# Performance work log

Hardware: AMD Instinct MI355X
Metric: run time of the kernel (lower is better)

Reference implementation:

```python
import jax, jax.numpy as jnp
import numpy as np

NEG_SLOPE = 0.2


def setup_inputs() -> dict:
    key = jax.random.key(0)
    ks = jax.random.split(key, 5)
    N, E, Din, Dout = 100000, 1600000, 64, 64
    x = jax.random.normal(ks[0], (N, Din), dtype=jnp.float32)
    edge_index = jax.random.randint(ks[1], (2, E), 0, N, dtype=jnp.int64)
    # Glorot-ish scale for weights
    W_l = jax.random.normal(ks[2], (Din, Dout), dtype=jnp.float32) / np.sqrt(Din)
    W_r = jax.random.normal(ks[3], (Din, Dout), dtype=jnp.float32) / np.sqrt(Din)
    att = jax.random.normal(ks[4], (Dout,), dtype=jnp.float32) / np.sqrt(Dout)
    bias = jnp.zeros((Dout,), dtype=jnp.float32)
    return {"x": x, "edge_index": edge_index, "W_l": W_l, "W_r": W_r, "att": att, "bias": bias}


def reference(x, edge_index, W_l, W_r, att, bias):
    N = x.shape[0]
    # PyG GATv2Conv default: add self loops
    loop = jnp.arange(N, dtype=edge_index.dtype)
    src = jnp.concatenate([edge_index[0], loop])  # j (source / message)
    dst = jnp.concatenate([edge_index[1], loop])  # i (target / aggregation)

    x_l = x @ W_l  # [N, Dout] source transform
    x_r = x @ W_r  # [N, Dout] target transform

    # per-edge attention logit: att . LeakyReLU(x_l[j] + x_r[i])
    e = jax.nn.leaky_relu(x_l[src] + x_r[dst], NEG_SLOPE) @ att  # [E+N]

    # segment softmax grouped by destination node
    e_max = jax.ops.segment_max(e, dst, num_segments=N)  # [N]
    e_exp = jnp.exp(e - e_max[dst])
    denom = jax.ops.segment_sum(e_exp, dst, num_segments=N)  # [N]
    alpha = e_exp / denom[dst]  # [E+N]

    # weighted scatter-add aggregation of source features
    out = jax.ops.segment_sum(alpha[:, None] * x_l[src], dst, num_segments=N)
    return out + bias
```

## Files before the change

### kernel.cpp

```cpp
#include <hip/hip_runtime.h>
#include <hip/hip_fp16.h>

#define NEG_SLOPE 0.2f
#define CH 4096
#define UN 16
#define BW 512
#define CAP2 10240
#define QCAP 2560

__global__ __launch_bounds__(256) void k_gemm(const float* __restrict__ x,
                                              const float* __restrict__ Wl,
                                              const float* __restrict__ Wr,
                                              __half* __restrict__ xl,
                                              __half* __restrict__ xr,
                                              int* __restrict__ bcount,
                                              int NB, int N) {
    __shared__ float sX[128 * 64];
    __shared__ float sW[64 * 128];
    const int t = threadIdx.x;
    const int B = blockIdx.x * 128;

    if (blockIdx.x == 0 && t < NB) bcount[t] = 0;

    for (int f = t; f < 2048; f += 256) {
        const int k = f >> 5, cg = f & 31;
        float4 v;
        if (cg < 16) v = reinterpret_cast<const float4*>(Wl)[k * 16 + cg];
        else         v = reinterpret_cast<const float4*>(Wr)[k * 16 + (cg - 16)];
        reinterpret_cast<float4*>(sW)[f] = v;
    }
    for (int f = t; f < 2048; f += 256) {
        const int r = B + (f >> 4);
        float4 v = {0.f, 0.f, 0.f, 0.f};
        if (r < N) v = reinterpret_cast<const float4*>(x)[(size_t)B * 16 + f];
        reinterpret_cast<float4*>(sX)[f] = v;
    }
    __syncthreads();

    const int cg = t & 31;
    const int g  = t >> 5;

    float4 acc[16];
#pragma unroll
    for (int i = 0; i < 16; i++) acc[i] = make_float4(0.f, 0.f, 0.f, 0.f);

    for (int kk = 0; kk < 64; kk += 4) {
        const float4 w0 = reinterpret_cast<const float4*>(sW)[(kk + 0) * 32 + cg];
        const float4 w1 = reinterpret_cast<const float4*>(sW)[(kk + 1) * 32 + cg];
        const float4 w2 = reinterpret_cast<const float4*>(sW)[(kk + 2) * 32 + cg];
        const float4 w3 = reinterpret_cast<const float4*>(sW)[(kk + 3) * 32 + cg];
#pragma unroll
        for (int i = 0; i < 16; i++) {
            const float4 xv = reinterpret_cast<const float4*>(sX)[(g * 16 + i) * 16 + (kk >> 2)];
            acc[i].x = fmaf(xv.x, w0.x, acc[i].x);
            acc[i].y = fmaf(xv.x, w0.y, acc[i].y);
            acc[i].z = fmaf(xv.x, w0.z, acc[i].z);
            acc[i].w = fmaf(xv.x, w0.w, acc[i].w);
            acc[i].x = fmaf(xv.y, w1.x, acc[i].x);
            acc[i].y = fmaf(xv.y, w1.y, acc[i].y);
            acc[i].z = fmaf(xv.y, w1.z, acc[i].z);
            acc[i].w = fmaf(xv.y, w1.w, acc[i].w);
            acc[i].x = fmaf(xv.z, w2.x, acc[i].x);
            acc[i].y = fmaf(xv.z, w2.y, acc[i].y);
            acc[i].z = fmaf(xv.z, w2.z, acc[i].z);
            acc[i].w = fmaf(xv.z, w2.w, acc[i].w);
            acc[i].x = fmaf(xv.w, w3.x, acc[i].x);
            acc[i].y = fmaf(xv.w, w3.y, acc[i].y);
            acc[i].z = fmaf(xv.w, w3.z, acc[i].z);
            acc[i].w = fmaf(xv.w, w3.w, acc[i].w);
        }
    }

    const int c = cg * 4;
    __half* dstp = (c < 64) ? (xl + c) : (xr + (c - 64));
#pragma unroll
    for (int i = 0; i < 16; i++) {
        const int r = B + g * 16 + i;
        if (r < N) {
            __half2 h01, h23;
            h01.x = __float2half_rn(acc[i].x);
            h01.y = __float2half_rn(acc[i].y);
            h23.x = __float2half_rn(acc[i].z);
            h23.y = __float2half_rn(acc[i].w);
            uint2 u;
            u.x = *reinterpret_cast<unsigned int*>(&h01);
            u.y = *reinterpret_cast<unsigned int*>(&h23);
            *reinterpret_cast<uint2*>(dstp + (size_t)r * 64) = u;
        }
    }
}

__global__ __launch_bounds__(256) void k_part(const int* __restrict__ src,
                                              const int* __restrict__ dst,
                                              int* __restrict__ bcount,
                                              int* __restrict__ part,
                                              int E, int M, int NB) {
    __shared__ int skey[CH];
    __shared__ unsigned char sbkt[CH];
    __shared__ int hist[256];
    __shared__ int lcur[256];
    __shared__ int gofs[256];
    const int t = threadIdx.x;
    const int b = blockIdx.x;
    const int lo = b * CH;
    const int cnt = min(M - lo, CH);

    hist[t] = 0;
    __syncthreads();

    int rs[UN], rd[UN];
#pragma unroll
    for (int u = 0; u < UN; u++) {
        const int k = lo + t + u * 256;
        rd[u] = -1; rs[u] = 0;
        if (k < M) {
            if (k < E) { rs[u] = src[k]; rd[u] = dst[k]; }
            else       { rs[u] = k - E;  rd[u] = rs[u]; }
        }
    }
#pragma unroll
    for (int u = 0; u < UN; u++)
        if (rd[u] >= 0) atomicAdd(&hist[rd[u] >> 9], 1);
    __syncthreads();

    const int h = hist[t];
    lcur[t] = h;
    __syncthreads();
    for (int o = 1; o < 256; o <<= 1) {
        const int v = (t >= o) ? lcur[t - o] : 0;
        __syncthreads();
        lcur[t] += v;
        __syncthreads();
    }
    const int ex = lcur[t] - h;
    int gbase = 0;
    if (t < NB && h > 0) gbase = atomicAdd(&bcount[t], h);
    __syncthreads();
    lcur[t] = ex;
    gofs[t] = t * CAP2 + gbase - ex;
    __syncthreads();

#pragma unroll
    for (int u = 0; u < UN; u++) {
        if (rd[u] >= 0) {
            const int bkt = rd[u] >> 9;
            const int p = atomicAdd(&lcur[bkt], 1);
            skey[p] = (rs[u] << 9) | (rd[u] & 511);
            sbkt[p] = (unsigned char)bkt;
        }
    }
    __syncthreads();

    for (int i = t; i < cnt; i += 256) {
        const int bkt = sbkt[i];
        const int pos = gofs[bkt] + i;
        if (pos - bkt * CAP2 < CAP2) part[pos] = skey[i];
    }
}

__global__ __launch_bounds__(256) void k_bsf(const int* __restrict__ part,
                                             const int* __restrict__ bcount,
                                             int* __restrict__ sedge,
                                             int* __restrict__ off,
                                             int* __restrict__ deg, int N) {
    __shared__ int skey[QCAP];
    __shared__ int outk[QCAP];
    __shared__ int lhist[128];
    __shared__ int loff[128];
    __shared__ int lcur[128];
    __shared__ int sh2[128];
    __shared__ int scnt;
    const int t = threadIdx.x;
    const int bkt = blockIdx.x >> 2;
    const int qt  = blockIdx.x & 3;
    const int base  = bkt * CAP2;
    const int qbase = base + qt * QCAP;
    const int n = min(bcount[bkt], CAP2);

    if (t == 0) scnt = 0;
    if (t < 128) lhist[t] = 0;
    __syncthreads();

    for (int i = t; i < n; i += 256) {
        const int k = part[base + i];
        const int dl = k & 511;
        if ((dl >> 7) == qt) {
            const int p = atomicAdd(&scnt, 1);
            if (p < QCAP) {
                skey[p] = k;
                atomicAdd(&lhist[dl & 127], 1);
            }
        }
    }
    __syncthreads();
    const int m = min(scnt, QCAP);

    if (t < 128) sh2[t] = lhist[t];
    __syncthreads();
    for (int o = 1; o < 128; o <<= 1) {
        int v = 0;
        if (t < 128 && t >= o) v = sh2[t - o];
        __syncthreads();
        if (t < 128) sh2[t] += v;
        __syncthreads();
    }
    if (t < 128) {
        const int ex = sh2[t] - lhist[t];
        loff[t] = ex;
        lcur[t] = ex;
        const int node = (bkt << 9) + (qt << 7) + t;
        if (node < N) { off[node] = qbase + ex; deg[node] = lhist[t]; }
    }
    __syncthreads();

    for (int i = t; i < m; i += 256) {
        const int k = skey[i];
        const int pos = atomicAdd(&lcur[k & 127], 1);
        outk[pos] = k >> 9;
    }
    __syncthreads();
    for (int i = t; i < m; i += 256) sedge[qbase + i] = outk[i];
}

__global__ void k_fused(const int* __restrict__ offv, const int* __restrict__ degv,
                        const int* __restrict__ sedge, const __half* __restrict__ xl,
                        const __half* __restrict__ xr, const float* __restrict__ att,
                        const float* __restrict__ bias, float* __restrict__ out, int N) {
    const int lane = threadIdx.x & 63;
    const int gl = lane & 15;
    const int q = lane >> 4;
    int wave = (blockIdx.x * blockDim.x + threadIdx.x) >> 6;
    const int nw = (gridDim.x * blockDim.x) >> 6;
    const float4 a = reinterpret_cast<const float4*>(att)[gl];
    const float4 b = reinterpret_cast<const float4*>(bias)[gl];
    for (int i = wave; i < N; i += nw) {
        const int base = offv[i];
        const int dg = degv[i];
        const uint2 xru = reinterpret_cast<const uint2*>(xr + (size_t)i * 64)[gl];
        const float2 r01 = __half22float2(*reinterpret_cast<const __half2*>(&xru.x));
        const float2 r23 = __half22float2(*reinterpret_cast<const __half2*>(&xru.y));
        float s = 0.f;
        float4 acc = {0.f, 0.f, 0.f, 0.f};
        int tt = q;
        for (; tt + 4 < dg; tt += 8) {
            const int j0 = sedge[base + tt];
            const int j1 = sedge[base + tt + 4];
            const uint2 xu0 = reinterpret_cast<const uint2*>(xl + (size_t)j0 * 64)[gl];
            const uint2 xu1 = reinterpret_cast<const uint2*>(xl + (size_t)j1 * 64)[gl];
            const float2 l01a = __half22float2(*reinterpret_cast<const __half2*>(&xu0.x));
            const float2 l23a = __half22float2(*reinterpret_cast<const __half2*>(&xu0.y));
            const float2 l01b = __half22float2(*reinterpret_cast<const __half2*>(&xu1.x));
            const float2 l23b = __half22float2(*reinterpret_cast<const __half2*>(&xu1.y));
            float v0 = l01a.x + r01.x; v0 = fmaxf(v0, NEG_SLOPE * v0);
            float v1 = l01a.y + r01.y; v1 = fmaxf(v1, NEG_SLOPE * v1);
            float v2 = l23a.x + r23.x; v2 = fmaxf(v2, NEG_SLOPE * v2);
            float v3 = l23a.y + r23.y; v3 = fmaxf(v3, NEG_SLOPE * v3);
            float u0 = l01b.x + r01.x; u0 = fmaxf(u0, NEG_SLOPE * u0);
            float u1 = l01b.y + r01.y; u1 = fmaxf(u1, NEG_SLOPE * u1);
            float u2 = l23b.x + r23.x; u2 = fmaxf(u2, NEG_SLOPE * u2);
            float u3 = l23b.y + r23.y; u3 = fmaxf(u3, NEG_SLOPE * u3);
            float p0 = a.x * v0 + a.y * v1 + a.z * v2 + a.w * v3;
            float p1 = a.x * u0 + a.y * u1 + a.z * u2 + a.w * u3;
            p0 += __shfl_xor(p0, 1, 16);
            p1 += __shfl_xor(p1, 1, 16);
            p0 += __shfl_xor(p0, 2, 16);
            p1 += __shfl_xor(p1, 2, 16);
            p0 += __shfl_xor(p0, 4, 16);
            p1 += __shfl_xor(p1, 4, 16);
            p0 += __shfl_xor(p0, 8, 16);
            p1 += __shfl_xor(p1, 8, 16);
            const float w0 = __expf(p0);
            const float w1 = __expf(p1);
            s += w0 + w1;
            acc.x = fmaf(w0, l01a.x, acc.x); acc.x = fmaf(w1, l01b.x, acc.x);
            acc.y = fmaf(w0, l01a.y, acc.y); acc.y = fmaf(w1, l01b.y, acc.y);
            acc.z = fmaf(w0, l23a.x, acc.z); acc.z = fmaf(w1, l23b.x, acc.z);
            acc.w = fmaf(w0, l23a.y, acc.w); acc.w = fmaf(w1, l23b.y, acc.w);
        }
        for (; tt < dg; tt += 4) {
            const int j = sedge[base + tt];
            const uint2 xu = reinterpret_cast<const uint2*>(xl + (size_t)j * 64)[gl];
            const float2 l01 = __half22float2(*reinterpret_cast<const __half2*>(&xu.x));
            const float2 l23 = __half22float2(*reinterpret_cast<const __half2*>(&xu.y));
            float v0 = l01.x + r01.x; v0 = fmaxf(v0, NEG_SLOPE * v0);
            float v1 = l01.y + r01.y; v1 = fmaxf(v1, NEG_SLOPE * v1);
            float v2 = l23.x + r23.x; v2 = fmaxf(v2, NEG_SLOPE * v2);
            float v3 = l23.y + r23.y; v3 = fmaxf(v3, NEG_SLOPE * v3);
            float p = a.x * v0 + a.y * v1 + a.z * v2 + a.w * v3;
            p += __shfl_xor(p, 1, 16);
            p += __shfl_xor(p, 2, 16);
            p += __shfl_xor(p, 4, 16);
            p += __shfl_xor(p, 8, 16);
            const float w = __expf(p);
            s += w;
            acc.x = fmaf(w, l01.x, acc.x);
            acc.y = fmaf(w, l01.y, acc.y);
            acc.z = fmaf(w, l23.x, acc.z);
            acc.w = fmaf(w, l23.y, acc.w);
        }
        s += __shfl_xor(s, 16); s += __shfl_xor(s, 32);
        acc.x += __shfl_xor(acc.x, 16); acc.x += __shfl_xor(acc.x, 32);
        acc.y += __shfl_xor(acc.y, 16); acc.y += __shfl_xor(acc.y, 32);
        acc.z += __shfl_xor(acc.z, 16); acc.z += __shfl_xor(acc.z, 32);
        acc.w += __shfl_xor(acc.w, 16); acc.w += __shfl_xor(acc.w, 32);
        if (q == 0) {
            const float inv = 1.f / s;
            float4 o;
            o.x = fmaf(acc.x, inv, b.x);
            o.y = fmaf(acc.y, inv, b.y);
            o.z = fmaf(acc.z, inv, b.z);
            o.w = fmaf(acc.w, inv, b.w);
            reinterpret_cast<float4*>(out)[(size_t)i * 16 + gl] = o;
        }
    }
}

extern "C" void kernel_launch(void* const* d_in, const int* in_sizes, int n_in,
                              void* d_out, int out_size, void* d_ws, size_t ws_size,
                              hipStream_t stream) {
    const float* x    = (const float*)d_in[0];
    const int*   ei   = (const int*)d_in[1];
    const float* Wl   = (const float*)d_in[2];
    const float* Wr   = (const float*)d_in[3];
    const float* att  = (const float*)d_in[4];
    const float* bias = (const float*)d_in[5];
    float* out = (float*)d_out;

    const int N = in_sizes[0] / 64;
    const int E = in_sizes[1] / 2;
    const int M = E + N;
    const int ng  = (N + 127) / 128;
    const int nch = (M + CH - 1) / CH;
    const int NB  = (N + BW - 1) / BW;

    __half* xl = (__half*)d_ws;
    __half* xr = xl + (size_t)N * 64;
    int* deg    = (int*)(xr + (size_t)N * 64);
    int* off    = deg + N;
    int* bcount = off + N;
    int* part   = bcount + NB;
    int* sedge  = part + (size_t)NB * CAP2;

    k_gemm<<<ng, 256, 0, stream>>>(x, Wl, Wr, xl, xr, bcount, NB, N);
    k_part<<<nch, 256, 0, stream>>>(ei, ei + E, bcount, part, E, M, NB);
    k_bsf<<<NB * 4, 256, 0, stream>>>(part, bcount, sedge, off, deg, N);
    k_fused<<<2048, 256, 0, stream>>>(off, deg, sedge, xl, xr, att, bias, out, N);
}
```

Before: 206.0 us.

## Merge GEMM and edge partition into one launch; warp-aggregate bucket-split atomics

The node-feature GEMM and the edge partition pass are merged into a single kernel that picks its role from the block index, with a shared 64KB buffer reused by both branches. The bucket counters are now zeroed with an async memset, since the partition blocks may run alongside the GEMM blocks. This lets two independent stages overlap and removes one launch boundary. In the bucket-split kernel, per-thread shared atomics on the key counter are replaced by a warp ballot with one atomic per warp. The cost is higher shared memory use for the partition blocks, which can lower their occupancy, plus an extra memset launch.

```diff
diff --git a/kernel.cpp b/kernel.cpp
--- a/kernel.cpp
+++ b/kernel.cpp
@@ -8,153 +8,151 @@
 #define CAP2 10240
 #define QCAP 2560
 
-__global__ __launch_bounds__(256) void k_gemm(const float* __restrict__ x,
-                                              const float* __restrict__ Wl,
-                                              const float* __restrict__ Wr,
-                                              __half* __restrict__ xl,
-                                              __half* __restrict__ xr,
-                                              int* __restrict__ bcount,
-                                              int NB, int N) {
-    __shared__ float sX[128 * 64];
-    __shared__ float sW[64 * 128];
+__global__ __launch_bounds__(256) void k_gp(const float* __restrict__ x,
+                                            const float* __restrict__ Wl,
+                                            const float* __restrict__ Wr,
+                                            __half* __restrict__ xl,
+                                            __half* __restrict__ xr,
+                                            const int* __restrict__ src,
+                                            const int* __restrict__ dst,
+                                            int* __restrict__ bcount,
+                                            int* __restrict__ part,
+                                            int E, int M, int NB, int ng, int N) {
+    __shared__ float smem[16384];
     const int t = threadIdx.x;
-    const int B = blockIdx.x * 128;
-
-    if (blockIdx.x == 0 && t < NB) bcount[t] = 0;
-
-    for (int f = t; f < 2048; f += 256) {
-        const int k = f >> 5, cg = f & 31;
-        float4 v;
-        if (cg < 16) v = reinterpret_cast<const float4*>(Wl)[k * 16 + cg];
-        else         v = reinterpret_cast<const float4*>(Wr)[k * 16 + (cg - 16)];
-        reinterpret_cast<float4*>(sW)[f] = v;
-    }
-    for (int f = t; f < 2048; f += 256) {
-        const int r = B + (f >> 4);
-        float4 v = {0.f, 0.f, 0.f, 0.f};
-        if (r < N) v = reinterpret_cast<const float4*>(x)[(size_t)B * 16 + f];
-        reinterpret_cast<float4*>(sX)[f] = v;
-    }
-    __syncthreads();
-
-    const int cg = t & 31;
-    const int g  = t >> 5;
-
-    float4 acc[16];
-#pragma unroll
-    for (int i = 0; i < 16; i++) acc[i] = make_float4(0.f, 0.f, 0.f, 0.f);
-
-    for (int kk = 0; kk < 64; kk += 4) {
-        const float4 w0 = reinterpret_cast<const float4*>(sW)[(kk + 0) * 32 + cg];
-        const float4 w1 = reinterpret_cast<const float4*>(sW)[(kk + 1) * 32 + cg];
-        const float4 w2 = reinterpret_cast<const float4*>(sW)[(kk + 2) * 32 + cg];
-        const float4 w3 = reinterpret_cast<const float4*>(sW)[(kk + 3) * 32 + cg];
+
+    if (blockIdx.x < ng) {
+        float* sX = smem;
+        float* sW = smem + 8192;
+        const int B = blockIdx.x * 128;
+
+        for (int f = t; f < 2048; f += 256) {
+            const int k = f >> 5, cg = f & 31;
+            float4 v;
+            if (cg < 16) v = reinterpret_cast<const float4*>(Wl)[k * 16 + cg];
+            else         v = reinterpret_cast<const float4*>(Wr)[k * 16 + (cg - 16)];
+            reinterpret_cast<float4*>(sW)[f] = v;
+        }
+        for (int f = t; f < 2048; f += 256) {
+            const int r = B + (f >> 4);
+            float4 v = {0.f, 0.f, 0.f, 0.f};
+            if (r < N) v = reinterpret_cast<const float4*>(x)[(size_t)B * 16 + f];
+            reinterpret_cast<float4*>(sX)[f] = v;
+        }
+        __syncthreads();
+
+        const int cg = t & 31;
+        const int g  = t >> 5;
+
+        float4 acc[16];
+#pragma unroll
+        for (int i = 0; i < 16; i++) acc[i] = make_float4(0.f, 0.f, 0.f, 0.f);
+
+        for (int kk = 0; kk < 64; kk += 4) {
+            const float4 w0 = reinterpret_cast<const float4*>(sW)[(kk + 0) * 32 + cg];
+            const float4 w1 = reinterpret_cast<const float4*>(sW)[(kk + 1) * 32 + cg];
+            const float4 w2 = reinterpret_cast<const float4*>(sW)[(kk + 2) * 32 + cg];
+            const float4 w3 = reinterpret_cast<const float4*>(sW)[(kk + 3) * 32 + cg];
+#pragma unroll
+            for (int i = 0; i < 16; i++) {
+                const float4 xv = reinterpret_cast<const float4*>(sX)[(g * 16 + i) * 16 + (kk >> 2)];
+                acc[i].x = fmaf(xv.x, w0.x, acc[i].x);
+                acc[i].y = fmaf(xv.x, w0.y, acc[i].y);
+                acc[i].z = fmaf(xv.x, w0.z, acc[i].z);
+                acc[i].w = fmaf(xv.x, w0.w, acc[i].w);
+                acc[i].x = fmaf(xv.y, w1.x, acc[i].x);
+                acc[i].y = fmaf(xv.y, w1.y, acc[i].y);
+                acc[i].z = fmaf(xv.y, w1.z, acc[i].z);
+                acc[i].w = fmaf(xv.y, w1.w, acc[i].w);
+                acc[i].x = fmaf(xv.z, w2.x, acc[i].x);
+                acc[i].y = fmaf(xv.z, w2.y, acc[i].y);
+                acc[i].z = fmaf(xv.z, w2.z, acc[i].z);
+                acc[i].w = fmaf(xv.z, w2.w, acc[i].w);
+                acc[i].x = fmaf(xv.w, w3.x, acc[i].x);
+                acc[i].y = fmaf(xv.w, w3.y, acc[i].y);
+                acc[i].z = fmaf(xv.w, w3.z, acc[i].z);
+                acc[i].w = fmaf(xv.w, w3.w, acc[i].w);
+            }
+        }
+
+        const int c = cg * 4;
+        __half* dstp = (c < 64) ? (xl + c) : (xr + (c - 64));
 #pragma unroll
         for (int i = 0; i < 16; i++) {
-            const float4 xv = reinterpret_cast<const float4*>(sX)[(g * 16 + i) * 16 + (kk >> 2)];
-            acc[i].x = fmaf(xv.x, w0.x, acc[i].x);
-            acc[i].y = fmaf(xv.x, w0.y, acc[i].y);
-            acc[i].z = fmaf(xv.x, w0.z, acc[i].z);
-            acc[i].w = fmaf(xv.x, w0.w, acc[i].w);
-            acc[i].x = fmaf(xv.y, w1.x, acc[i].x);
-            acc[i].y = fmaf(xv.y, w1.y, acc[i].y);
-            acc[i].z = fmaf(xv.y, w1.z, acc[i].z);
-            acc[i].w = fmaf(xv.y, w1.w, acc[i].w);
-            acc[i].x = fmaf(xv.z, w2.x, acc[i].x);
-            acc[i].y = fmaf(xv.z, w2.y, acc[i].y);
-            acc[i].z = fmaf(xv.z, w2.z, acc[i].z);
-            acc[i].w = fmaf(xv.z, w2.w, acc[i].w);
-            acc[i].x = fmaf(xv.w, w3.x, acc[i].x);
-            acc[i].y = fmaf(xv.w, w3.y, acc[i].y);
-            acc[i].z = fmaf(xv.w, w3.z, acc[i].z);
-            acc[i].w = fmaf(xv.w, w3.w, acc[i].w);
-        }
-    }
-
-    const int c = cg * 4;
-    __half* dstp = (c < 64) ? (xl + c) : (xr + (c - 64));
-#pragma unroll
-    for (int i = 0; i < 16; i++) {
-        const int r = B + g * 16 + i;
-        if (r < N) {
-            __half2 h01, h23;
-            h01.x = __float2half_rn(acc[i].x);
-            h01.y = __float2half_rn(acc[i].y);
-            h23.x = __float2half_rn(acc[i].z);
-            h23.y = __float2half_rn(acc[i].w);
-            uint2 u;
-            u.x = *reinterpret_cast<unsigned int*>(&h01);
-            u.y = *reinterpret_cast<unsigned int*>(&h23);
-            *reinterpret_cast<uint2*>(dstp + (size_t)r * 64) = u;
-        }
-    }
-}
-
-__global__ __launch_bounds__(256) void k_part(const int* __restrict__ src,
-                                              const int* __restrict__ dst,
-                                              int* __restrict__ bcount,
-                                              int* __restrict__ part,
-                                              int E, int M, int NB) {
-    __shared__ int skey[CH];
-    __shared__ unsigned char sbkt[CH];
-    __shared__ int hist[256];
-    __shared__ int lcur[256];
-    __shared__ int gofs[256];
-    const int t = threadIdx.x;
-    const int b = blockIdx.x;
-    const int lo = b * CH;
-    const int cnt = min(M - lo, CH);
-
-    hist[t] = 0;
-    __syncthreads();
-
-    int rs[UN], rd[UN];
-#pragma unroll
-    for (int u = 0; u < UN; u++) {
-        const int k = lo + t + u * 256;
-        rd[u] = -1; rs[u] = 0;
-        if (k < M) {
-            if (k < E) { rs[u] = src[k]; rd[u] = dst[k]; }
-            else       { rs[u] = k - E;  rd[u] = rs[u]; }
-        }
-    }
-#pragma unroll
-    for (int u = 0; u < UN; u++)
-        if (rd[u] >= 0) atomicAdd(&hist[rd[u] >> 9], 1);
-    __syncthreads();
-
-    const int h = hist[t];
-    lcur[t] = h;
-    __syncthreads();
-    for (int o = 1; o < 256; o <<= 1) {
-        const int v = (t >= o) ? lcur[t - o] : 0;
-        __syncthreads();
-        lcur[t] += v;
-        __syncthreads();
-    }
-    const int ex = lcur[t] - h;
-    int gbase = 0;
-    if (t < NB && h > 0) gbase = atomicAdd(&bcount[t], h);
-    __syncthreads();
-    lcur[t] = ex;
-    gofs[t] = t * CAP2 + gbase - ex;
-    __syncthreads();
-
-#pragma unroll
-    for (int u = 0; u < UN; u++) {
-        if (rd[u] >= 0) {
-            const int bkt = rd[u] >> 9;
-            const int p = atomicAdd(&lcur[bkt], 1);
-            skey[p] = (rs[u] << 9) | (rd[u] & 511);
-            sbkt[p] = (unsigned char)bkt;
-        }
-    }
-    __syncthreads();
-
-    for (int i = t; i < cnt; i += 256) {
-        const int bkt = sbkt[i];
-        const int pos = gofs[bkt] + i;
-        if (pos - bkt * CAP2 < CAP2) part[pos] = skey[i];
+            const int r = B + g * 16 + i;
+            if (r < N) {
+                __half2 h01, h23;
+                h01.x = __float2half_rn(acc[i].x);
+                h01.y = __float2half_rn(acc[i].y);
+                h23.x = __float2half_rn(acc[i].z);
+                h23.y = __float2half_rn(acc[i].w);
+                uint2 u;
+                u.x = *reinterpret_cast<unsigned int*>(&h01);
+                u.y = *reinterpret_cast<unsigned int*>(&h23);
+                *reinterpret_cast<uint2*>(dstp + (size_t)r * 64) = u;
+            }
+        }
+    } else {
+        int* skey = (int*)smem;
+        unsigned char* sbkt = (unsigned char*)(smem + 4096);
+        int* hist = (int*)smem + 5120;
+        int* lcur = (int*)smem + 5376;
+        int* gofs = (int*)smem + 5632;
+        const int b = blockIdx.x - ng;
+        const int lo = b * CH;
+        const int cnt = min(M - lo, CH);
+
+        hist[t] = 0;
+        __syncthreads();
+
+        int rs[UN], rd[UN];
+#pragma unroll
+        for (int u = 0; u < UN; u++) {
+            const int k = lo + t + u * 256;
+            rd[u] = -1; rs[u] = 0;
+            if (k < M) {
+                if (k < E) { rs[u] = src[k]; rd[u] = dst[k]; }
+                else       { rs[u] = k - E;  rd[u] = rs[u]; }
+            }
+        }
+#pragma unroll
+        for (int u = 0; u < UN; u++)
+            if (rd[u] >= 0) atomicAdd(&hist[rd[u] >> 9], 1);
+        __syncthreads();
+
+        const int h = hist[t];
+        lcur[t] = h;
+        __syncthreads();
+        for (int o = 1; o < 256; o <<= 1) {
+            const int v = (t >= o) ? lcur[t - o] : 0;
+            __syncthreads();
+            lcur[t] += v;
+            __syncthreads();
+        }
+        const int ex = lcur[t] - h;
+        int gbase = 0;
+        if (t < NB && h > 0) gbase = atomicAdd(&bcount[t], h);
+        __syncthreads();
+        lcur[t] = ex;
+        gofs[t] = t * CAP2 + gbase - ex;
+        __syncthreads();
+
+#pragma unroll
+        for (int u = 0; u < UN; u++) {
+            if (rd[u] >= 0) {
+                const int bkt = rd[u] >> 9;
+                const int p = atomicAdd(&lcur[bkt], 1);
+                skey[p] = (rs[u] << 9) | (rd[u] & 511);
+                sbkt[p] = (unsigned char)bkt;
+            }
+        }
+        __syncthreads();
+
+        for (int i = t; i < cnt; i += 256) {
+            const int bkt = sbkt[i];
+            const int pos = gofs[bkt] + i;
+            if (pos - bkt * CAP2 < CAP2) part[pos] = skey[i];
+        }
     }
 }
 
@@ -169,31 +167,45 @@
     __shared__ int loff[128];
     __shared__ int lcur[128];
     __shared__ int sh2[128];
-    __shared__ int scnt;
+    __shared__ int kcnt;
     const int t = threadIdx.x;
+    const int lane = t & 63;
     const int bkt = blockIdx.x >> 2;
     const int qt  = blockIdx.x & 3;
     const int base  = bkt * CAP2;
     const int qbase = base + qt * QCAP;
     const int n = min(bcount[bkt], CAP2);
 
-    if (t == 0) scnt = 0;
+    if (t == 0) kcnt = 0;
     if (t < 128) lhist[t] = 0;
     __syncthreads();
 
-    for (int i = t; i < n; i += 256) {
-        const int k = part[base + i];
-        const int dl = k & 511;
-        if ((dl >> 7) == qt) {
-            const int p = atomicAdd(&scnt, 1);
-            if (p < QCAP) {
-                skey[p] = k;
-                atomicAdd(&lhist[dl & 127], 1);
-            }
-        }
-    }
-    __syncthreads();
-    const int m = min(scnt, QCAP);
+    const int rounds = (n + 255) >> 8;
+    for (int r = 0; r < rounds; ++r) {
+        const int i = (r << 8) + t;
+        int k = 0;
+        bool m = false;
+        if (i < n) {
+            k = part[base + i];
+            m = (((k >> 7) & 3) == qt);
+        }
+        const unsigned long long bal = __ballot(m);
+        if (bal) {
+            const int leader = __ffsll(bal) - 1;
+            int b2 = 0;
+            if (lane == leader) b2 = atomicAdd(&kcnt, __popcll(bal));
+            b2 = __shfl(b2, leader);
+            if (m) {
+                const int p = b2 + __popcll(bal & ((1ull << lane) - 1));
+                if (p < QCAP) {
+                    skey[p] = k;
+                    atomicAdd(&lhist[k & 127], 1);
+                }
+            }
+        }
+    }
+    __syncthreads();
+    const int m = min(kcnt, QCAP);
 
     if (t < 128) sh2[t] = lhist[t];
     __syncthreads();
@@ -341,8 +353,9 @@
     int* part   = bcount + NB;
     int* sedge  = part + (size_t)NB * CAP2;
 
-    k_gemm<<<ng, 256, 0, stream>>>(x, Wl, Wr, xl, xr, bcount, NB, N);
-    k_part<<<nch, 256, 0, stream>>>(ei, ei + E, bcount, part, E, M, NB);
+    hipMemsetAsync(bcount, 0, (size_t)NB * sizeof(int), stream);
+    k_gp<<<ng + nch, 256, 0, stream>>>(x, Wl, Wr, xl, xr, ei, ei + E,
+                                       bcount, part, E, M, NB, ng, N);
     k_bsf<<<NB * 4, 256, 0, stream>>>(part, bcount, sedge, off, deg, N);
     k_fused<<<2048, 256, 0, stream>>>(off, deg, sedge, xl, xr, att, bias, out, N);
 }
```

Measured after the change: 198.0 us. -3.9%, faster.
